# Performance work log

Hardware: AMD Instinct MI355X
Metric: run time of the kernel (lower is better)

## Reference

```python
import jax, jax.numpy as jnp
import numpy as np

LOG2PI = float(np.log(2.0 * np.pi))
CLIP_LO, CLIP_HI = 1e-6, 1.0 - 1e-6


def gaussian_log_prob(X, mu):
    # X: (s, d), mu: (K, d) -> (s, K); unit-variance diagonal Normal.
    d = X.shape[-1]
    sq = (
        (X * X).sum(-1, keepdims=True)
        - 2.0 * (X @ mu.T)
        + (mu * mu).sum(-1)[None, :]
    )
    return -0.5 * (sq + d * LOG2PI)


def setup_inputs() -> dict:
    key = jax.random.key(0)
    kz, ks, kd, km1, km2 = jax.random.split(key, 5)
    s, K, n, dz = 60000, 200, 6, 64
    Z = jax.random.normal(kz, (s, dz), dtype=jnp.float32)
    S = jax.random.normal(ks, (s, 3), dtype=jnp.float32)
    D = jax.random.randint(kd, (s, n), 0, s, dtype=jnp.int64)
    sel_mu = jax.random.normal(km1, (K, dz), dtype=jnp.float32)
    spa_mu = jax.random.normal(km2, (K, 3), dtype=jnp.float32)
    return {"Z": Z, "S": S, "D": D, "sel_mu": sel_mu, "spa_mu": spa_mu}


def reference(Z, S, D, sel_mu, spa_mu):
    # point energy U: (s, K)
    U = -(gaussian_log_prob(Z, sel_mu) + gaussian_log_prob(S, spa_mu))
    Q = jax.nn.softmax(-U, axis=-1)  # temperature = 1.0
    # expected point energy: (s,)
    point = (Q * U).sum(-1)
    # doublet energy: gather neighbor rows, coassignment, potential, mask
    Qc = jnp.clip(Q, CLIP_LO, CLIP_HI)
    co = jnp.einsum('snk,sk->sn', Qc[D], Qc)  # (s, n)
    doublet = jnp.where(D < 0, 0.0, -jnp.log(co)).sum(-1)  # (s,)
    return point + doublet
```

## Files before the change

kernel.cpp:

```cpp
#include <hip/hip_runtime.h>
#include <hip/hip_fp16.h>
#include <math.h>

#define KK 200
#define NT 13
#define NNB 6
#define Q8STRIDE 256

typedef __attribute__((ext_vector_type(8))) short short8;
typedef __attribute__((ext_vector_type(4))) float f32x4;
typedef _Float16 half2v __attribute__((ext_vector_type(2)));
typedef __fp16 fp16x2 __attribute__((ext_vector_type(2)));
#define MFMA16 __builtin_amdgcn_mfma_f32_16x16x32_bf16

union U8 { short8 s; uint4 u; };
union H2U { half2v h; unsigned u; };
union P2U { fp16x2 h; unsigned u; };

__device__ __forceinline__ unsigned short bfh(float f) {
    unsigned u = __float_as_uint(f);
    return (unsigned short)((u + 0x7fffu + ((u >> 16) & 1u)) >> 16);
}
__device__ __forceinline__ float bf2f(unsigned short h) {
    return __uint_as_float(((unsigned)h) << 16);
}
__device__ __forceinline__ short8 z8() {
    short8 v;
#pragma unroll
    for (int j = 0; j < 8; ++j) v[j] = 0;
    return v;
}
__device__ __forceinline__ void cvp(float f0, float f1, unsigned& hw, unsigned& lw) {
    unsigned u0 = __float_as_uint(f0), u1 = __float_as_uint(f1);
    float l0 = f0 - __uint_as_float(u0 & 0xffff0000u);
    float l1 = f1 - __uint_as_float(u1 & 0xffff0000u);
    hw = __builtin_amdgcn_perm(u1, u0, 0x07060302u);
    lw = __builtin_amdgcn_perm(__float_as_uint(l1), __float_as_uint(l0), 0x07060302u);
}
__device__ __forceinline__ unsigned e5pair_lo(unsigned w) {
    return __builtin_amdgcn_perm(w, 0u, 0x05000400u);
}
__device__ __forceinline__ unsigned e5pair_hi(unsigned w) {
    return __builtin_amdgcn_perm(w, 0u, 0x07000600u);
}
__device__ __forceinline__ half2v as_h2(unsigned u) { H2U x; x.u = u; return x.h; }
__device__ __forceinline__ unsigned pkrtz_u(float a, float b) {
    P2U x; x.h = __builtin_amdgcn_cvt_pkrtz(a, b); return x.u;
}
#define DPP_ROR_ADD(t, ctrl)                                                        \
    t += __int_as_float(__builtin_amdgcn_update_dpp(0, __float_as_int(t), (ctrl),   \
                                                    0xF, 0xF, true))

__global__ __launch_bounds__(512, 4) void
k_point(const float* __restrict__ Z, const float* __restrict__ S,
        const float* __restrict__ selmu, const float* __restrict__ spamu,
        unsigned char* __restrict__ Qc8, float* __restrict__ pointbuf,
        int sRows, int mTiles)
{
    __shared__ short8 ldsBh[26 * 64];
    __shared__ short8 ldsBl[26 * 64];
    __shared__ uint2  ldsB2h[NT * 16];
    __shared__ uint2  ldsB2l[NT * 16];
    __shared__ float  normAcc[NT * 16];

    const int tid = threadIdx.x;

    if (tid < NT * 16) normAcc[tid] = 0.f;
    __syncthreads();

    for (int slot = tid; slot < 26 * 64; slot += 512) {
        int L = slot & 63, ts = slot >> 6;
        int t = ts >> 1, sstep = ts & 1;
        int n = t * 16 + (L & 15);
        int kb = sstep * 32 + (L >> 4) * 8;
        U8 hi, lo;
        hi.s = z8(); lo.s = z8();
        if (n < KK) {
            const float* mp = selmu + (size_t)n * 64 + kb;
            float4 a = *(const float4*)mp;
            float4 b = *(const float4*)(mp + 4);
            cvp(a.x, a.y, hi.u.x, lo.u.x);
            cvp(a.z, a.w, hi.u.y, lo.u.y);
            cvp(b.x, b.y, hi.u.z, lo.u.z);
            cvp(b.z, b.w, hi.u.w, lo.u.w);
            float ss = a.x*a.x + a.y*a.y + a.z*a.z + a.w*a.w
                     + b.x*b.x + b.y*b.y + b.z*b.z + b.w*b.w;
            atomicAdd(&normAcc[n], ss);
        }
        ldsBh[slot] = hi.s;
        ldsBl[slot] = lo.s;
    }
    __syncthreads();
    if (tid < NT * 16) {
        int n = tid;
        uint2 vh = make_uint2(0, 0), vl = make_uint2(0, 0);
        if (n < KK) {
            float p0 = spamu[n * 3 + 0], p1 = spamu[n * 3 + 1], p2 = spamu[n * 3 + 2];
            float nrm = -0.5f * (normAcc[n] + p0 * p0 + p1 * p1 + p2 * p2);
            unsigned short h0 = bfh(p0), h1 = bfh(p1), h2 = bfh(p2), h3 = bfh(nrm);
            unsigned short g0 = bfh(p0 - bf2f(h0)), g1 = bfh(p1 - bf2f(h1));
            unsigned short g2 = bfh(p2 - bf2f(h2)), g3 = bfh(nrm - bf2f(h3));
            vh = make_uint2((unsigned)h0 | ((unsigned)h1 << 16), (unsigned)h2 | ((unsigned)h3 << 16));
            vl = make_uint2((unsigned)g0 | ((unsigned)g1 << 16), (unsigned)g2 | ((unsigned)g3 << 16));
        }
        ldsB2h[tid] = vh;
        ldsB2l[tid] = vl;
    }
    __syncthreads();

    const int wave = tid >> 6;
    const int lane = tid & 63;
    const int q = lane >> 4;
    const int li = lane & 15;
    const float cLog = 0.5f * 67.0f * 1.8378770664093453f;

    const int tile = blockIdx.x * 8 + wave;
    if (tile >= mTiles) return;
    const int m0 = tile * 16;
    const int row = m0 + li;
    const int rowA = (row < sRows) ? row : (sRows - 1);

    const float* zr = Z + (size_t)rowA * 64 + q * 8;
    float4 z0 = *(const float4*)zr;
    float4 z1 = *(const float4*)(zr + 4);
    float4 z2 = *(const float4*)(zr + 32);
    float4 z3 = *(const float4*)(zr + 36);
    U8 ah0, al0, ah1, al1;
    cvp(z0.x, z0.y, ah0.u.x, al0.u.x);
    cvp(z0.z, z0.w, ah0.u.y, al0.u.y);
    cvp(z1.x, z1.y, ah0.u.z, al0.u.z);
    cvp(z1.z, z1.w, ah0.u.w, al0.u.w);
    cvp(z2.x, z2.y, ah1.u.x, al1.u.x);
    cvp(z2.z, z2.w, ah1.u.y, al1.u.y);
    cvp(z3.x, z3.y, ah1.u.z, al1.u.z);
    cvp(z3.z, z3.w, ah1.u.w, al1.u.w);

    float zz = z0.x*z0.x + z0.y*z0.y + z0.z*z0.z + z0.w*z0.w
             + z1.x*z1.x + z1.y*z1.y + z1.z*z1.z + z1.w*z1.w
             + z2.x*z2.x + z2.y*z2.y + z2.z*z2.z + z2.w*z2.w
             + z3.x*z3.x + z3.y*z3.y + z3.z*z3.z + z3.w*z3.w;
    zz += __shfl_xor(zz, 16);
    zz += __shfl_xor(zz, 32);

    float s0v = S[(size_t)rowA * 3 + 0];
    float s1v = S[(size_t)rowA * 3 + 1];
    float s2v = S[(size_t)rowA * 3 + 2];
    float cz = 0.5f * (zz + s0v * s0v + s1v * s1v + s2v * s2v) + cLog;

    U8 rsh, rsl;
    rsh.s = z8(); rsl.s = z8();
    if (lane < 16) {
        cvp(s0v, s1v, rsh.u.x, rsl.u.x);
        unsigned hw, lw;
        cvp(s2v, 1.0f, hw, lw);
        rsh.u.y = hw;
        rsl.u.y = lw & 0x0000ffffu;
    }

    f32x4 acc[NT];
#pragma unroll
    for (int t = 0; t < NT; ++t) { f32x4 zv = {0.f, 0.f, 0.f, 0.f}; acc[t] = zv; }

#pragma unroll
    for (int t = 0; t < NT; ++t) {
        short8 b0 = ldsBh[(t * 2 + 0) * 64 + lane];
        short8 b1 = ldsBh[(t * 2 + 1) * 64 + lane];
        short8 c0 = ldsBl[(t * 2 + 0) * 64 + lane];
        short8 c1 = ldsBl[(t * 2 + 1) * 64 + lane];
        uint2 bh2 = make_uint2(0, 0), bl2 = make_uint2(0, 0);
        if (lane < 16) { bh2 = ldsB2h[t * 16 + lane]; bl2 = ldsB2l[t * 16 + lane]; }
        U8 cmh, cml;
        cmh.s = z8(); cml.s = z8();
        cmh.u.x = bh2.x; cmh.u.y = bh2.y;
        cml.u.x = bl2.x; cml.u.y = bl2.y;

        acc[t] = MFMA16(b0, ah0.s, acc[t], 0, 0, 0);
        acc[t] = MFMA16(b1, ah1.s, acc[t], 0, 0, 0);
        acc[t] = MFMA16(b0, al0.s, acc[t], 0, 0, 0);
        acc[t] = MFMA16(b1, al1.s, acc[t], 0, 0, 0);
        acc[t] = MFMA16(c0, ah0.s, acc[t], 0, 0, 0);
        acc[t] = MFMA16(c1, ah1.s, acc[t], 0, 0, 0);
        acc[t] = MFMA16(cmh.s, rsh.s, acc[t], 0, 0, 0);
        acc[t] = MFMA16(cmh.s, rsl.s, acc[t], 0, 0, 0);
        acc[t] = MFMA16(cml.s, rsh.s, acc[t], 0, 0, 0);
    }

    const bool padQ = (q >= 2);
    float mx = -1e30f;
#pragma unroll
    for (int t = 0; t < NT; ++t) {
#pragma unroll
        for (int r = 0; r < 4; ++r) {
            float v = acc[t][r];
            if (t == 12 && padQ) v = -1e30f;
            acc[t][r] = v;
            mx = fmaxf(mx, v);
        }
    }
    mx = fmaxf(mx, __shfl_xor(mx, 16));
    mx = fmaxf(mx, __shfl_xor(mx, 32));
    float sl = 0.f, pl = 0.f;
#pragma unroll
    for (int t = 0; t < NT; ++t) {
#pragma unroll
        for (int r = 0; r < 4; ++r) {
            float v = acc[t][r];
            float ee = __expf(v - mx);
            sl += ee;
            pl = fmaf(ee, v, pl);
            acc[t][r] = ee;
        }
    }
    sl += __shfl_xor(sl, 16);
    sl += __shfl_xor(sl, 32);
    pl += __shfl_xor(pl, 16);
    pl += __shfl_xor(pl, 32);
    float inv = 1.0f / sl;

    if (row < sRows) {
        unsigned char* qp = Qc8 + (size_t)row * Q8STRIDE + q * 4;
#pragma unroll
        for (int t = 0; t < NT; ++t) {
            unsigned w = 0;
            if (t < 12 || !padQ) {
                float c0 = fminf(fmaxf(acc[t][0] * inv, 1e-6f), 1.0f - 1e-6f) * 1024.0f;
                float c1 = fminf(fmaxf(acc[t][1] * inv, 1e-6f), 1.0f - 1e-6f) * 1024.0f;
                float c2 = fminf(fmaxf(acc[t][2] * inv, 1e-6f), 1.0f - 1e-6f) * 1024.0f;
                float c3 = fminf(fmaxf(acc[t][3] * inv, 1e-6f), 1.0f - 1e-6f) * 1024.0f;
                unsigned ua = pkrtz_u(c0, c1);
                unsigned ub = pkrtz_u(c2, c3);
                unsigned t0 = ua + 0x007f007fu + ((ua >> 8) & 0x00010001u);
                unsigned t1 = ub + 0x007f007fu + ((ub >> 8) & 0x00010001u);
                w = __builtin_amdgcn_perm(t1, t0, 0x07050301u);
            }
            *(unsigned*)(qp + t * 16) = w;
        }
        *(unsigned*)(qp + 13 * 16) = 0u;
        *(unsigned*)(qp + 14 * 16) = 0u;
        *(unsigned*)(qp + 15 * 16) = 0u;
        if (lane < 16) pointbuf[row] = cz - pl * inv;
    }
}

__global__ __launch_bounds__(512, 8) void
k_doublet(const unsigned char* __restrict__ Qc8, const float* __restrict__ pointbuf,
          const int* __restrict__ D, float* __restrict__ out, int sRows)
{
    const int lane = threadIdx.x & 63;
    const int wave = threadIdx.x >> 6;
    const int g = lane >> 4;
    const int l16 = lane & 15;
    const int row = blockIdx.x * 32 + wave * 4 + g;
    if (row >= sRows) return;

    const float LN2_20 = 13.862943611198906f;

    const int* dp = D + (size_t)row * NNB;
    int2 d01 = *(const int2*)dp;
    int2 d23 = *(const int2*)(dp + 2);
    int2 d45 = *(const int2*)(dp + 4);
    const int dj[6] = { d01.x, d01.y, d23.x, d23.y, d45.x, d45.y };

    const unsigned off = (unsigned)l16 * 16u;
    uint4 ow = *(const uint4*)(Qc8 + (size_t)row * Q8STRIDE + off);
    uint4 nb[NNB];
#pragma unroll
    for (int j = 0; j < NNB; ++j) {
        int dd = (dj[j] >= 0) ? dj[j] : row;
        nb[j] = *(const uint4*)(Qc8 + (size_t)dd * Q8STRIDE + off);
    }

    unsigned o0 = e5pair_lo(ow.x), o1 = e5pair_hi(ow.x);
    unsigned o2 = e5pair_lo(ow.y), o3 = e5pair_hi(ow.y);
    unsigned o4 = e5pair_lo(ow.z), o5 = e5pair_hi(ow.z);
    unsigned o6 = e5pair_lo(ow.w), o7 = e5pair_hi(ow.w);

    float dbl = 0.f;
#pragma unroll
    for (int j = 0; j < NNB; ++j) {
        float t = 0.f;
#if __has_builtin(__builtin_amdgcn_fdot2)
        t = __builtin_amdgcn_fdot2(as_h2(o0), as_h2(e5pair_lo(nb[j].x)), t, false);
        t = __builtin_amdgcn_fdot2(as_h2(o1), as_h2(e5pair_hi(nb[j].x)), t, false);
        t = __builtin_amdgcn_fdot2(as_h2(o2), as_h2(e5pair_lo(nb[j].y)), t, false);
        t = __builtin_amdgcn_fdot2(as_h2(o3), as_h2(e5pair_hi(nb[j].y)), t, false);
        t = __builtin_amdgcn_fdot2(as_h2(o4), as_h2(e5pair_lo(nb[j].z)), t, false);
        t = __builtin_amdgcn_fdot2(as_h2(o5), as_h2(e5pair_hi(nb[j].z)), t, false);
        t = __builtin_amdgcn_fdot2(as_h2(o6), as_h2(e5pair_lo(nb[j].w)), t, false);
        t = __builtin_amdgcn_fdot2(as_h2(o7), as_h2(e5pair_hi(nb[j].w)), t, false);
#else
        {
            unsigned ov[8] = { o0, o1, o2, o3, o4, o5, o6, o7 };
            unsigned bv[8] = { e5pair_lo(nb[j].x), e5pair_hi(nb[j].x),
                               e5pair_lo(nb[j].y), e5pair_hi(nb[j].y),
                               e5pair_lo(nb[j].z), e5pair_hi(nb[j].z),
                               e5pair_lo(nb[j].w), e5pair_hi(nb[j].w) };
#pragma unroll
            for (int k = 0; k < 8; ++k) {
                half2v a = as_h2(ov[k]), b = as_h2(bv[k]);
                t = fmaf((float)a[0], (float)b[0], t);
                t = fmaf((float)a[1], (float)b[1], t);
            }
        }
#endif
        DPP_ROR_ADD(t, 0x128);
        DPP_ROR_ADD(t, 0x124);
        DPP_ROR_ADD(t, 0x122);
        DPP_ROR_ADD(t, 0x121);
        if (dj[j] >= 0) dbl += LN2_20 - __logf(t);
    }

    if (l16 == 0) out[row] = pointbuf[row] + dbl;
}

extern "C" void kernel_launch(void* const* d_in, const int* in_sizes, int n_in,
                              void* d_out, int out_size, void* d_ws, size_t ws_size,
                              hipStream_t stream) {
    const float* Z     = (const float*)d_in[0];
    const float* S     = (const float*)d_in[1];
    const int*   D     = (const int*)d_in[2];
    const float* selmu = (const float*)d_in[3];
    const float* spamu = (const float*)d_in[4];
    float* out = (float*)d_out;
    const int s = out_size;

    unsigned char* Qc8 = (unsigned char*)d_ws;
    float* pointbuf = (float*)((char*)d_ws + (size_t)s * Q8STRIDE);

    const int mTiles = (s + 15) / 16;
    const int grid1 = (mTiles + 7) / 8;
    k_point<<<grid1, 512, 0, stream>>>(Z, S, selmu, spamu, Qc8, pointbuf, s, mTiles);

    const int grid2 = (s + 31) / 32;
    k_doublet<<<grid2, 512, 0, stream>>>(Qc8, pointbuf, D, out, s);
}
```

Baseline: 101.7 us.

## Compute doublet coassignment dot products with bf8 MFMA instead of fdot2

Rewrites the doublet kernel so each wave handles a 16-row tile and computes the 16x16 self-by-neighbor products for each neighbor slot with 16x16x32 bf8 MFMA, taking only the diagonal entries. It replaces the per-row packed fdot2 loop and the DPP cross-lane reductions. The next neighbor's rows are software-prefetched while the current MFMAs run. This computes 16x more products than needed (only the diagonal is used) and changes occupancy and launch bounds.

```diff
diff --git a/kernel.cpp b/kernel.cpp
--- a/kernel.cpp
+++ b/kernel.cpp
@@ -12,9 +12,9 @@
 typedef _Float16 half2v __attribute__((ext_vector_type(2)));
 typedef __fp16 fp16x2 __attribute__((ext_vector_type(2)));
 #define MFMA16 __builtin_amdgcn_mfma_f32_16x16x32_bf16
+#define MFMA8  __builtin_amdgcn_mfma_f32_16x16x32_bf8_bf8
 
 union U8 { short8 s; uint4 u; };
-union H2U { half2v h; unsigned u; };
 union P2U { fp16x2 h; unsigned u; };
 
 __device__ __forceinline__ unsigned short bfh(float f) {
@@ -37,19 +37,9 @@
     hw = __builtin_amdgcn_perm(u1, u0, 0x07060302u);
     lw = __builtin_amdgcn_perm(__float_as_uint(l1), __float_as_uint(l0), 0x07060302u);
 }
-__device__ __forceinline__ unsigned e5pair_lo(unsigned w) {
-    return __builtin_amdgcn_perm(w, 0u, 0x05000400u);
-}
-__device__ __forceinline__ unsigned e5pair_hi(unsigned w) {
-    return __builtin_amdgcn_perm(w, 0u, 0x07000600u);
-}
-__device__ __forceinline__ half2v as_h2(unsigned u) { H2U x; x.u = u; return x.h; }
 __device__ __forceinline__ unsigned pkrtz_u(float a, float b) {
     P2U x; x.h = __builtin_amdgcn_cvt_pkrtz(a, b); return x.u;
 }
-#define DPP_ROR_ADD(t, ctrl)                                                        \
-    t += __int_as_float(__builtin_amdgcn_update_dpp(0, __float_as_int(t), (ctrl),   \
-                                                    0xF, 0xF, true))
 
 __global__ __launch_bounds__(512, 4) void
 k_point(const float* __restrict__ Z, const float* __restrict__ S,
@@ -242,75 +232,69 @@
     }
 }
 
-__global__ __launch_bounds__(512, 8) void
+__global__ __launch_bounds__(512, 4) void
 k_doublet(const unsigned char* __restrict__ Qc8, const float* __restrict__ pointbuf,
-          const int* __restrict__ D, float* __restrict__ out, int sRows)
+          const int* __restrict__ D, float* __restrict__ out, int sRows, int mTiles)
 {
     const int lane = threadIdx.x & 63;
     const int wave = threadIdx.x >> 6;
-    const int g = lane >> 4;
-    const int l16 = lane & 15;
-    const int row = blockIdx.x * 32 + wave * 4 + g;
-    if (row >= sRows) return;
-
+    const int q = lane >> 4;
+    const int li = lane & 15;
+    const int tile = blockIdx.x * 8 + wave;
+    if (tile >= mTiles) return;
+    const int m0 = tile * 16;
+    const int rowL = m0 + li;
+    const int rowC = (rowL < sRows) ? rowL : (sRows - 1);
     const float LN2_20 = 13.862943611198906f;
 
-    const int* dp = D + (size_t)row * NNB;
+    const int* dp = D + (size_t)rowC * NNB;
     int2 d01 = *(const int2*)dp;
     int2 d23 = *(const int2*)(dp + 2);
     int2 d45 = *(const int2*)(dp + 4);
     const int dj[6] = { d01.x, d01.y, d23.x, d23.y, d45.x, d45.y };
 
-    const unsigned off = (unsigned)l16 * 16u;
-    uint4 ow = *(const uint4*)(Qc8 + (size_t)row * Q8STRIDE + off);
-    uint4 nb[NNB];
+    const unsigned char* orow = Qc8 + (size_t)rowC * Q8STRIDE + q * 8;
+    long long a[8];
+#pragma unroll
+    for (int s = 0; s < 8; ++s) a[s] = *(const long long*)(orow + s * 32);
+
+    f32x4 acc[NNB];
+#pragma unroll
+    for (int j = 0; j < NNB; ++j) { f32x4 zv = {0.f, 0.f, 0.f, 0.f}; acc[j] = zv; }
+
+    long long b[8], bn[8];
+    {
+        int dd = (dj[0] >= 0) ? dj[0] : rowC;
+        const unsigned char* nrow = Qc8 + (size_t)dd * Q8STRIDE + q * 8;
+#pragma unroll
+        for (int s = 0; s < 8; ++s) b[s] = *(const long long*)(nrow + s * 32);
+    }
 #pragma unroll
     for (int j = 0; j < NNB; ++j) {
-        int dd = (dj[j] >= 0) ? dj[j] : row;
-        nb[j] = *(const uint4*)(Qc8 + (size_t)dd * Q8STRIDE + off);
-    }
-
-    unsigned o0 = e5pair_lo(ow.x), o1 = e5pair_hi(ow.x);
-    unsigned o2 = e5pair_lo(ow.y), o3 = e5pair_hi(ow.y);
-    unsigned o4 = e5pair_lo(ow.z), o5 = e5pair_hi(ow.z);
-    unsigned o6 = e5pair_lo(ow.w), o7 = e5pair_hi(ow.w);
-
-    float dbl = 0.f;
-#pragma unroll
-    for (int j = 0; j < NNB; ++j) {
-        float t = 0.f;
-#if __has_builtin(__builtin_amdgcn_fdot2)
-        t = __builtin_amdgcn_fdot2(as_h2(o0), as_h2(e5pair_lo(nb[j].x)), t, false);
-        t = __builtin_amdgcn_fdot2(as_h2(o1), as_h2(e5pair_hi(nb[j].x)), t, false);
-        t = __builtin_amdgcn_fdot2(as_h2(o2), as_h2(e5pair_lo(nb[j].y)), t, false);
-        t = __builtin_amdgcn_fdot2(as_h2(o3), as_h2(e5pair_hi(nb[j].y)), t, false);
-        t = __builtin_amdgcn_fdot2(as_h2(o4), as_h2(e5pair_lo(nb[j].z)), t, false);
-        t = __builtin_amdgcn_fdot2(as_h2(o5), as_h2(e5pair_hi(nb[j].z)), t, false);
-        t = __builtin_amdgcn_fdot2(as_h2(o6), as_h2(e5pair_lo(nb[j].w)), t, false);
-        t = __builtin_amdgcn_fdot2(as_h2(o7), as_h2(e5pair_hi(nb[j].w)), t, false);
-#else
-        {
-            unsigned ov[8] = { o0, o1, o2, o3, o4, o5, o6, o7 };
-            unsigned bv[8] = { e5pair_lo(nb[j].x), e5pair_hi(nb[j].x),
-                               e5pair_lo(nb[j].y), e5pair_hi(nb[j].y),
-                               e5pair_lo(nb[j].z), e5pair_hi(nb[j].z),
-                               e5pair_lo(nb[j].w), e5pair_hi(nb[j].w) };
-#pragma unroll
-            for (int k = 0; k < 8; ++k) {
-                half2v a = as_h2(ov[k]), b = as_h2(bv[k]);
-                t = fmaf((float)a[0], (float)b[0], t);
-                t = fmaf((float)a[1], (float)b[1], t);
-            }
-        }
-#endif
-        DPP_ROR_ADD(t, 0x128);
-        DPP_ROR_ADD(t, 0x124);
-        DPP_ROR_ADD(t, 0x122);
-        DPP_ROR_ADD(t, 0x121);
-        if (dj[j] >= 0) dbl += LN2_20 - __logf(t);
-    }
-
-    if (l16 == 0) out[row] = pointbuf[row] + dbl;
+        if (j < NNB - 1) {
+            int dd = (dj[j + 1] >= 0) ? dj[j + 1] : rowC;
+            const unsigned char* nrow = Qc8 + (size_t)dd * Q8STRIDE + q * 8;
+#pragma unroll
+            for (int s = 0; s < 8; ++s) bn[s] = *(const long long*)(nrow + s * 32);
+        }
+#pragma unroll
+        for (int s = 0; s < 8; ++s)
+            acc[j] = MFMA8((long)a[s], (long)b[s], acc[j], 0, 0, 0);
+#pragma unroll
+        for (int s = 0; s < 8; ++s) b[s] = bn[s];
+    }
+
+    if ((li >> 2) == q) {
+        const int r = li & 3;
+        float dbl = 0.f;
+#pragma unroll
+        for (int j = 0; j < NNB; ++j) {
+            float p = (r == 0) ? acc[j][0] : (r == 1) ? acc[j][1]
+                    : (r == 2) ? acc[j][2] : acc[j][3];
+            if (dj[j] >= 0) dbl += LN2_20 - __logf(p);
+        }
+        if (rowL < sRows) out[rowL] = pointbuf[rowL] + dbl;
+    }
 }
 
 extern "C" void kernel_launch(void* const* d_in, const int* in_sizes, int n_in,
@@ -331,6 +315,5 @@
     const int grid1 = (mTiles + 7) / 8;
     k_point<<<grid1, 512, 0, stream>>>(Z, S, selmu, spamu, Qc8, pointbuf, s, mTiles);
 
-    const int grid2 = (s + 31) / 32;
-    k_doublet<<<grid2, 512, 0, stream>>>(Qc8, pointbuf, D, out, s);
-}
+    k_doublet<<<grid1, 512, 0, stream>>>(Qc8, pointbuf, D, out, s, mTiles);
+}
```

Result: slower. 114.6 us (+12.7%).
